# Performance work log

Measured on AMD Instinct MI355X. Metric: run time of the kernel, lower is better.

## Reference

```python
import jax, jax.numpy as jnp
import numpy as np

B, T, C = 2, 2048, 1024
NH, NKV, HD = 16, 4, 64
VEC = 32  # ve_gate_channels


def _rope(x, cos, sin):
    d = x.shape[-1] // 2
    x1, x2 = x[..., :d], x[..., d:]
    return jnp.concatenate([x1 * cos + x2 * sin, -x1 * sin + x2 * cos], axis=-1)


def _rmsnorm(x):
    eps = jnp.finfo(x.dtype).eps
    return x * jax.lax.rsqrt(jnp.mean(x * x, axis=-1, keepdims=True) + eps)


def setup_inputs() -> dict:
    key = jax.random.key(0)
    ks = jax.random.split(key, 9)
    s = 0.02
    return {
        "x": jax.random.normal(ks[0], (B, T, C), jnp.float32),
        "ve": jax.random.normal(ks[1], (B, T, NKV * HD), jnp.float32),
        "cos": jax.random.normal(ks[2], (1, T, 1, HD // 2), jnp.float32),
        "sin": jax.random.normal(ks[3], (1, T, 1, HD // 2), jnp.float32),
        "Wq": jax.random.normal(ks[4], (C, NH * HD), jnp.float32) * s,
        "Wk": jax.random.normal(ks[5], (C, NKV * HD), jnp.float32) * s,
        "Wv": jax.random.normal(ks[6], (C, NKV * HD), jnp.float32) * s,
        "Wproj": jax.random.normal(ks[7], (C, C), jnp.float32) * s,
        "Wgate": jax.random.normal(ks[8], (VEC, NKV), jnp.float32) * s,
        "window_size": 1024,
    }


def reference(x, ve, cos, sin, Wq, Wk, Wv, Wproj, Wgate, window_size):
    Bx, Tx, Cx = x.shape
    q = (x @ Wq).reshape(Bx, Tx, NH, HD)
    k = (x @ Wk).reshape(Bx, Tx, NKV, HD)
    v = (x @ Wv).reshape(Bx, Tx, NKV, HD)

    # value-embedding gate (has_ve True for this layer)
    gate = 2.0 * jax.nn.sigmoid(x[..., :VEC] @ Wgate)  # [B,T,NKV]
    v = v + gate[..., None] * ve.reshape(Bx, Tx, NKV, HD)

    q, k = _rope(q, cos, sin), _rope(k, cos, sin)
    q, k = _rmsnorm(q), _rmsnorm(k)

    q = q.transpose(0, 2, 1, 3)  # [B,NH,T,HD]
    k = k.transpose(0, 2, 1, 3)  # [B,NKV,T,HD]
    v = v.transpose(0, 2, 1, 3)

    # GQA: each KV head serves NH//NKV consecutive q heads
    g = NH // NKV
    k = jnp.repeat(k, g, axis=1)
    v = jnp.repeat(v, g, axis=1)

    row = jnp.arange(Tx)[:, None]
    col = jnp.arange(Tx)[None, :]
    mask = (col <= row) & (col >= row - window_size)  # causal sliding window

    scores = jnp.einsum("bhqd,bhkd->bhqk", q, k) / np.sqrt(HD).astype(np.float32)
    scores = jnp.where(mask[None, None], scores, jnp.finfo(scores.dtype).min)
    attn = jax.nn.softmax(scores, axis=-1)
    y = jnp.einsum("bhqk,bhkd->bhqd", attn, v)

    y = y.transpose(0, 2, 1, 3).reshape(Bx, Tx, Cx)
    return y @ Wproj
```

## Files before the change

### kernel.cpp

```cpp
#include <hip/hip_runtime.h>

typedef __bf16 bf16x8 __attribute__((ext_vector_type(8)));
typedef __bf16 bf16x4 __attribute__((ext_vector_type(4)));
typedef float f32x4 __attribute__((ext_vector_type(4)));

__device__ inline float tof(float v) { return v; }
__device__ inline float tof(__bf16 v) { return (float)v; }

__device__ inline bf16x8 load8(const __bf16* p) { return *(const bf16x8*)p; }
__device__ inline bf16x8 load8(const float* p) {
    const float4 a = *(const float4*)p;
    const float4 b = *(const float4*)(p + 4);
    bf16x8 r;
    r[0] = (__bf16)a.x; r[1] = (__bf16)a.y; r[2] = (__bf16)a.z; r[3] = (__bf16)a.w;
    r[4] = (__bf16)b.x; r[5] = (__bf16)b.y; r[6] = (__bf16)b.z; r[7] = (__bf16)b.w;
    return r;
}

__device__ __forceinline__ void cp16(__bf16* lds, const __bf16* g) {
    __builtin_amdgcn_global_load_lds((__attribute__((address_space(1))) void*)g,
                                     (__attribute__((address_space(3))) void*)lds,
                                     16, 0, 0);
}

__global__ void sniff_kernel(const unsigned short* __restrict__ xs, int* flag) {
    int tid = threadIdx.x;
    int bad = 0;
    for (int i = tid; i < 512; i += 64) {
        unsigned int f = ((unsigned int)xs[i]) << 16;
        float v = __uint_as_float(f);
        float a = fabsf(v);
        if (!(a <= 1e4f) || (a != 0.f && a < 1e-6f)) bad++;
    }
    bad += __shfl_xor(bad, 1);  bad += __shfl_xor(bad, 2);
    bad += __shfl_xor(bad, 4);  bad += __shfl_xor(bad, 8);
    bad += __shfl_xor(bad, 16); bad += __shfl_xor(bad, 32);
    if (tid == 0) *flag = (bad > 32) ? 1 : 0;
}

template <typename T>
__device__ __forceinline__ void prep_body(
    const T* __restrict__ x, const T* __restrict__ ve,
    const T* __restrict__ cosp, const T* __restrict__ sinp,
    const T* __restrict__ Wq, const T* __restrict__ Wk,
    const T* __restrict__ Wv, const T* __restrict__ Wp, const T* __restrict__ Wg,
    __bf16* __restrict__ xb, __bf16* __restrict__ veb,
    float* __restrict__ cosf_, float* __restrict__ sinf_,
    __bf16* __restrict__ WqT, __bf16* __restrict__ WkT,
    __bf16* __restrict__ WvT, __bf16* __restrict__ WpT,
    __bf16* __restrict__ wgb, __bf16* tile)
{
    const int b = blockIdx.x, tid = threadIdx.x;

    if (b < 2625) {
        int g = b * 256 + tid;
        if (g < 524288) {
            *(bf16x8*)(xb + (size_t)g * 8) = load8(x + (size_t)g * 8);
        } else if (g < 655360) {
            int gg = g - 524288;
            *(bf16x8*)(veb + (size_t)gg * 8) = load8(ve + (size_t)gg * 8);
        } else if (g < 663552) {
            int gg = g - 655360;
            const T* s = cosp + (size_t)gg * 8; float* d = cosf_ + (size_t)gg * 8;
#pragma unroll
            for (int j = 0; j < 8; ++j) d[j] = tof(s[j]);
        } else if (g < 671744) {
            int gg = g - 663552;
            const T* s = sinp + (size_t)gg * 8; float* d = sinf_ + (size_t)gg * 8;
#pragma unroll
            for (int j = 0; j < 8; ++j) d[j] = tof(s[j]);
        } else if (g < 671760) {
            int gg = g - 671744;
            const T* s = Wg + (size_t)gg * 8; __bf16* d = wgb + (size_t)gg * 8;
#pragma unroll
            for (int j = 0; j < 8; ++j) d[j] = (__bf16)tof(s[j]);
        }
    } else {
        int idx = b - 2625;
        const T* src; __bf16* dst; int C;
        if (idx < 256)      { src = Wq; dst = WqT; C = 1024; }
        else if (idx < 320) { src = Wk; dst = WkT; C = 256;  idx -= 256; }
        else if (idx < 384) { src = Wv; dst = WvT; C = 256;  idx -= 320; }
        else                { src = Wp; dst = WpT; C = 1024; idx -= 384; }
        const int ctiles = C >> 6;
        const int r0 = (idx / ctiles) * 64, c0 = (idx % ctiles) * 64;
#pragma unroll
        for (int i = 0; i < 2; ++i) {
            int c = tid + i * 256, ir = c >> 3, ic = (c & 7) * 8;
            *(bf16x8*)(&tile[ir * 72 + ic]) = load8(src + (size_t)(r0 + ir) * C + c0 + ic);
        }
        __syncthreads();
#pragma unroll
        for (int i = 0; i < 2; ++i) {
            int c = tid + i * 256, orr = c >> 3, okc = (c & 7) * 8;
            bf16x8 v;
#pragma unroll
            for (int j = 0; j < 8; ++j) v[j] = tile[(okc + j) * 72 + orr];
            *(bf16x8*)(dst + (size_t)(c0 + orr) * 1024 + r0 + okc) = v;
        }
    }
}

__global__ __launch_bounds__(256) void prep_kernel(
    const void* x, const void* ve, const void* cosp, const void* sinp,
    const void* Wq, const void* Wk, const void* Wv, const void* Wp, const void* Wg,
    __bf16* xb, __bf16* veb, float* cosf_, float* sinf_,
    __bf16* WqT, __bf16* WkT, __bf16* WvT, __bf16* WpT,
    __bf16* wgb, const int* __restrict__ flag)
{
    __shared__ __bf16 tile[64 * 72];
    if (*flag) {
        prep_body<float>((const float*)x, (const float*)ve, (const float*)cosp,
                         (const float*)sinp, (const float*)Wq, (const float*)Wk,
                         (const float*)Wv, (const float*)Wp, (const float*)Wg,
                         xb, veb, cosf_, sinf_, WqT, WkT, WvT, WpT, wgb, tile);
    } else {
        prep_body<__bf16>((const __bf16*)x, (const __bf16*)ve, (const __bf16*)cosp,
                          (const __bf16*)sinp, (const __bf16*)Wq, (const __bf16*)Wk,
                          (const __bf16*)Wv, (const __bf16*)Wp, (const __bf16*)Wg,
                          xb, veb, cosf_, sinf_, WqT, WkT, WvT, WpT, wgb, tile);
    }
}

__global__ __launch_bounds__(256) void qkv_kernel(
    const __bf16* __restrict__ xb,
    const __bf16* __restrict__ WqT, const __bf16* __restrict__ WkT,
    const __bf16* __restrict__ WvT, const __bf16* __restrict__ veb,
    const float* __restrict__ cosf_, const float* __restrict__ sinf_,
    const __bf16* __restrict__ wgb,
    __bf16* __restrict__ qo, __bf16* __restrict__ ko, __bf16* __restrict__ vTo)
{
    const int row0 = blockIdx.x * 128;
    const int cb = blockIdx.y;
    const __bf16* BT; int col0, h, mode;
    if (cb < 16)      { BT = WqT; col0 = cb * 64;        h = cb;      mode = 0; }
    else if (cb < 20) { BT = WkT; col0 = (cb - 16) * 64; h = cb - 16; mode = 1; }
    else              { BT = WvT; col0 = (cb - 20) * 64; h = cb - 20; mode = 2; }

    __shared__ __align__(16) __bf16 As[2][128 * 32];
    __shared__ __align__(16) __bf16 Bs[2][64 * 32];

    const int tid  = threadIdx.x;
    const int w    = tid >> 6;
    const int lane = tid & 63;
    const int quad = lane >> 4;
    const int l15  = lane & 15;
    const int wr   = w * 32;

    f32x4 acc[2][4];
#pragma unroll
    for (int mi = 0; mi < 2; ++mi)
#pragma unroll
        for (int nj = 0; nj < 4; ++nj) acc[mi][nj] = (f32x4){0.f, 0.f, 0.f, 0.f};

    bf16x8 wgB;
#pragma unroll
    for (int j = 0; j < 8; ++j) wgB[j] = (__bf16)0.f;
    if (mode == 2 && l15 < 4) {
#pragma unroll
        for (int j = 0; j < 8; ++j) wgB[j] = wgb[(quad * 8 + j) * 4 + l15];
    }
    f32x4 zacc[2];
    zacc[0] = (f32x4){0.f, 0.f, 0.f, 0.f};
    zacc[1] = (f32x4){0.f, 0.f, 0.f, 0.f};

    auto stage = [&](int buf, int kk) {
#pragma unroll
        for (int i = 0; i < 2; ++i) {
            int c = i * 256 + tid;
            cp16(&As[buf][c * 8], &xb[(size_t)(row0 + (c >> 2)) * 1024 + kk + ((c & 3) << 3)]);
        }
        cp16(&Bs[buf][tid * 8], &BT[(size_t)(col0 + (tid >> 2)) * 1024 + kk + ((tid & 3) << 3)]);
    };

    stage(0, 0);
    __syncthreads();

    for (int kk = 0; kk < 1024; kk += 32) {
        const int cur = (kk >> 5) & 1;
        if (kk + 32 < 1024) stage(cur ^ 1, kk + 32);

        bf16x8 a[2], bfr[4];
#pragma unroll
        for (int mi = 0; mi < 2; ++mi) a[mi]  = *(const bf16x8*)(&As[cur][(wr + mi * 16 + l15) * 32 + quad * 8]);
#pragma unroll
        for (int nj = 0; nj < 4; ++nj) bfr[nj] = *(const bf16x8*)(&Bs[cur][(nj * 16 + l15) * 32 + quad * 8]);
        if (mode == 2 && kk == 0) {
            zacc[0] = __builtin_amdgcn_mfma_f32_16x16x32_bf16(a[0], wgB, zacc[0], 0, 0, 0);
            zacc[1] = __builtin_amdgcn_mfma_f32_16x16x32_bf16(a[1], wgB, zacc[1], 0, 0, 0);
        }
#pragma unroll
        for (int mi = 0; mi < 2; ++mi)
#pragma unroll
            for (int nj = 0; nj < 4; ++nj)
                acc[mi][nj] = __builtin_amdgcn_mfma_f32_16x16x32_bf16(a[mi], bfr[nj], acc[mi][nj], 0, 0, 0);
        __syncthreads();
    }

    if (mode < 2) {
        __bf16* dst = (mode == 0) ? qo : ko;
        const int nh = (mode == 0) ? 16 : 4;
#pragma unroll
        for (int mi = 0; mi < 2; ++mi) {
#pragma unroll
            for (int r = 0; r < 4; ++r) {
                int row = row0 + wr + mi * 16 + quad * 4 + r;
                int b = row >> 11, t = row & 2047;
                float c0 = cosf_[t * 32 + l15];
                float c1 = cosf_[t * 32 + 16 + l15];
                float s0 = sinf_[t * 32 + l15];
                float s1 = sinf_[t * 32 + 16 + l15];
                float v0 =  c0 * acc[mi][0][r] + s0 * acc[mi][2][r];
                float v1 =  c1 * acc[mi][1][r] + s1 * acc[mi][3][r];
                float v2 = -s0 * acc[mi][0][r] + c0 * acc[mi][2][r];
                float v3 = -s1 * acc[mi][1][r] + c1 * acc[mi][3][r];
                float ss = v0 * v0 + v1 * v1 + v2 * v2 + v3 * v3;
                ss += __shfl_xor(ss, 1); ss += __shfl_xor(ss, 2);
                ss += __shfl_xor(ss, 4); ss += __shfl_xor(ss, 8);
                float sc = rsqrtf(ss * (1.f / 64.f) + 1.1920929e-7f);
                size_t base = (((size_t)b * nh + h) * 2048 + t) * 64;
                dst[base + 0 * 16 + l15] = (__bf16)(v0 * sc);
                dst[base + 1 * 16 + l15] = (__bf16)(v1 * sc);
                dst[base + 2 * 16 + l15] = (__bf16)(v2 * sc);
                dst[base + 3 * 16 + l15] = (__bf16)(v3 * sc);
            }
        }
    } else {
#pragma unroll
        for (int mi = 0; mi < 2; ++mi) {
            int rowb = row0 + wr + mi * 16 + quad * 4;
            int b = rowb >> 11, t0 = rowb & 2047;
            float gg[4];
#pragma unroll
            for (int r = 0; r < 4; ++r) {
                float zv = __shfl(zacc[mi][r], quad * 16 + h);
                gg[r] = 2.f / (1.f + __expf(-zv));
            }
#pragma unroll
            for (int nj = 0; nj < 4; ++nj) {
                int d = nj * 16 + l15;
                bf16x4 pack;
#pragma unroll
                for (int r = 0; r < 4; ++r) {
                    int row = rowb + r;
                    float val = acc[mi][nj][r] + gg[r] * tof(veb[(size_t)row * 256 + h * 64 + d]);
                    pack[r] = (__bf16)val;
                }
                size_t a = (((size_t)b * 4 + h) * 64 + d) * 2048 + t0;
                *(bf16x4*)(&vTo[a]) = pack;
            }
        }
    }
}

__global__ __launch_bounds__(256) void attn_kernel(
    const __bf16* __restrict__ qg, const __bf16* __restrict__ kg,
    const __bf16* __restrict__ vTg, __bf16* __restrict__ yo,
    const int* __restrict__ winp)
{
    const int q0 = blockIdx.x * 128;
    const int hh = blockIdx.y, b = blockIdx.z;
    const int kvh = hh >> 2;
    const int W = winp[0];

    const int tid  = threadIdx.x;
    const int w    = tid >> 6;
    const int lane = tid & 63;
    const int quad = lane >> 4;
    const int l15  = lane & 15;

    __shared__ __align__(16) __bf16 Ks[2][64 * 64];
    __shared__ __align__(16) __bf16 Vt[2][64 * 64];
    __shared__ __align__(16) __bf16 Ps[4][32 * 72];

    bf16x8 qf[2][2];
#pragma unroll
    for (int i = 0; i < 2; ++i) {
        size_t qb = (((size_t)b * 16 + hh) * 2048 + q0 + w * 32 + i * 16 + l15) * 64;
        qf[i][0] = *(const bf16x8*)(&qg[qb + quad * 8]);
        qf[i][1] = *(const bf16x8*)(&qg[qb + 32 + quad * 8]);
    }

    f32x4 oacc[2][4];
    float lsum[2][4];
#pragma unroll
    for (int i = 0; i < 2; ++i)
#pragma unroll
        for (int n = 0; n < 4; ++n) {
            oacc[i][n] = (f32x4){0.f, 0.f, 0.f, 0.f};
            lsum[i][n] = 0.f;
        }

    const int lo = q0 - W;
    const int kt_lo = lo > 0 ? (lo >> 6) : 0;
    const int kt_hi = (q0 + 127) >> 6;
    const size_t kvbase = ((size_t)b * 4 + kvh) * 2048 * 64;

    auto stage = [&](int buf, int k0) {
#pragma unroll
        for (int i = 0; i < 2; ++i) {
            int c = i * 256 + tid;
            int rr = c >> 3;
            int jj = (c & 7) ^ (rr & 7);
            cp16(&Ks[buf][c * 8], &kg[kvbase + (size_t)(k0 + rr) * 64 + jj * 8]);
            cp16(&Vt[buf][c * 8], &vTg[kvbase + (size_t)rr * 2048 + k0 + jj * 8]);
        }
    };

    stage(0, kt_lo * 64);
    __syncthreads();

    int cur = 0;
    for (int kt = kt_lo; kt <= kt_hi; ++kt) {
        const int k0 = kt * 64;
        const bool need_mask = (k0 + 63 > q0) || (q0 + 127 - k0 > W);
        if (kt < kt_hi) stage(cur ^ 1, k0 + 64);

        f32x4 sacc[2][4];
#pragma unroll
        for (int i = 0; i < 2; ++i)
#pragma unroll
            for (int n = 0; n < 4; ++n) sacc[i][n] = (f32x4){0.f, 0.f, 0.f, 0.f};
        const __bf16* Kc = &Ks[cur][0];
#pragma unroll
        for (int n = 0; n < 4; ++n) {
            int m = n * 16 + l15;
            bf16x8 b0 = *(const bf16x8*)(&Kc[m * 64 + (quad ^ (m & 7)) * 8]);
            bf16x8 b1 = *(const bf16x8*)(&Kc[m * 64 + ((4 + quad) ^ (m & 7)) * 8]);
#pragma unroll
            for (int i = 0; i < 2; ++i) {
                sacc[i][n] = __builtin_amdgcn_mfma_f32_16x16x32_bf16(qf[i][0], b0, sacc[i][n], 0, 0, 0);
                sacc[i][n] = __builtin_amdgcn_mfma_f32_16x16x32_bf16(qf[i][1], b1, sacc[i][n], 0, 0, 0);
            }
        }

#pragma unroll
        for (int i = 0; i < 2; ++i) {
#pragma unroll
            for (int r = 0; r < 4; ++r) {
                const int row_g = q0 + w * 32 + i * 16 + quad * 4 + r;
#pragma unroll
                for (int n = 0; n < 4; ++n) {
                    float p = exp2f(fmaf(sacc[i][n][r], 0.18033688f, -11.5415603f));
                    if (need_mask) {
                        int col_g = k0 + n * 16 + l15;
                        bool ok = (col_g <= row_g) && (row_g - col_g <= W);
                        p = ok ? p : 0.f;
                    }
                    lsum[i][r] += p;
                    Ps[w][(i * 16 + quad * 4 + r) * 72 + n * 16 + l15] = (__bf16)p;
                }
            }
        }
        asm volatile("s_waitcnt lgkmcnt(0)" ::: "memory");

        const __bf16* Vc = &Vt[cur][0];
#pragma unroll
        for (int ks = 0; ks < 2; ++ks) {
            bf16x8 pfr0 = *(const bf16x8*)(&Ps[w][l15 * 72 + ks * 32 + quad * 8]);
            bf16x8 pfr1 = *(const bf16x8*)(&Ps[w][(16 + l15) * 72 + ks * 32 + quad * 8]);
#pragma unroll
            for (int n = 0; n < 4; ++n) {
                int m = n * 16 + l15;
                bf16x8 bv = *(const bf16x8*)(&Vc[m * 64 + ((ks * 4 + quad) ^ (m & 7)) * 8]);
                oacc[0][n] = __builtin_amdgcn_mfma_f32_16x16x32_bf16(pfr0, bv, oacc[0][n], 0, 0, 0);
                oacc[1][n] = __builtin_amdgcn_mfma_f32_16x16x32_bf16(pfr1, bv, oacc[1][n], 0, 0, 0);
            }
        }

        __syncthreads();
        cur ^= 1;
    }

#pragma unroll
    for (int i = 0; i < 2; ++i) {
#pragma unroll
        for (int r = 0; r < 4; ++r) {
            float l = lsum[i][r];
            l += __shfl_xor(l, 1); l += __shfl_xor(l, 2);
            l += __shfl_xor(l, 4); l += __shfl_xor(l, 8);
            float inv = 1.f / l;
            int t = q0 + w * 32 + i * 16 + quad * 4 + r;
            size_t base = ((size_t)(b * 2048 + t)) * 1024 + hh * 64;
#pragma unroll
            for (int n = 0; n < 4; ++n)
                yo[base + n * 16 + l15] = (__bf16)(oacc[i][n][r] * inv);
        }
    }
}

__global__ __launch_bounds__(256) void proj_kernel(
    const __bf16* __restrict__ y, const __bf16* __restrict__ WpT,
    void* __restrict__ outp, const int* __restrict__ flag)
{
    const int isf32 = *flag;
    const int row0 = blockIdx.x * 128;
    const int col0 = blockIdx.y * 64;
    __shared__ __align__(16) __bf16 As[2][128 * 32];
    __shared__ __align__(16) __bf16 Bs[2][64 * 32];

    const int tid  = threadIdx.x;
    const int w    = tid >> 6;
    const int lane = tid & 63;
    const int quad = lane >> 4;
    const int l15  = lane & 15;
    const int wr   = w * 32;

    f32x4 acc[2][4];
#pragma unroll
    for (int mi = 0; mi < 2; ++mi)
#pragma unroll
        for (int nj = 0; nj < 4; ++nj) acc[mi][nj] = (f32x4){0.f, 0.f, 0.f, 0.f};

    auto stage = [&](int buf, int kk) {
#pragma unroll
        for (int i = 0; i < 2; ++i) {
            int c = i * 256 + tid;
            cp16(&As[buf][c * 8], &y[(size_t)(row0 + (c >> 2)) * 1024 + kk + ((c & 3) << 3)]);
        }
        cp16(&Bs[buf][tid * 8], &WpT[(size_t)(col0 + (tid >> 2)) * 1024 + kk + ((tid & 3) << 3)]);
    };

    stage(0, 0);
    __syncthreads();

    for (int kk = 0; kk < 1024; kk += 32) {
        const int cur = (kk >> 5) & 1;
        if (kk + 32 < 1024) stage(cur ^ 1, kk + 32);

        bf16x8 a[2], bfr[4];
#pragma unroll
        for (int mi = 0; mi < 2; ++mi) a[mi]  = *(const bf16x8*)(&As[cur][(wr + mi * 16 + l15) * 32 + quad * 8]);
#pragma unroll
        for (int nj = 0; nj < 4; ++nj) bfr[nj] = *(const bf16x8*)(&Bs[cur][(nj * 16 + l15) * 32 + quad * 8]);
#pragma unroll
        for (int mi = 0; mi < 2; ++mi)
#pragma unroll
            for (int nj = 0; nj < 4; ++nj)
                acc[mi][nj] = __builtin_amdgcn_mfma_f32_16x16x32_bf16(a[mi], bfr[nj], acc[mi][nj], 0, 0, 0);
        __syncthreads();
    }

#pragma unroll
    for (int mi = 0; mi < 2; ++mi)
#pragma unroll
        for (int r = 0; r < 4; ++r) {
            int row = row0 + wr + mi * 16 + quad * 4 + r;
            if (isf32) {
                float* out = (float*)outp;
#pragma unroll
                for (int nj = 0; nj < 4; ++nj)
                    out[(size_t)row * 1024 + col0 + nj * 16 + l15] = acc[mi][nj][r];
            } else {
                __bf16* out = (__bf16*)outp;
#pragma unroll
                for (int nj = 0; nj < 4; ++nj)
                    out[(size_t)row * 1024 + col0 + nj * 16 + l15] = (__bf16)acc[mi][nj][r];
            }
        }
}

extern "C" void kernel_launch(void* const* d_in, const int* in_sizes, int n_in,
                              void* d_out, int out_size, void* d_ws, size_t ws_size,
                              hipStream_t stream) {
    const int* win = (const int*)d_in[9];

    char* p = (char*)d_ws;
    int*    flag = (int*)p;                    p += 256;
    __bf16* q_ws = (__bf16*)p;                 p += (size_t)4194304 * 2;
    __bf16* k_ws = (__bf16*)p;                 p += (size_t)1048576 * 2;
    __bf16* vT_ws= (__bf16*)p;                 p += (size_t)1048576 * 2;
    __bf16* y_ws = (__bf16*)p;                 p += (size_t)4194304 * 2;
    __bf16* xb   = (__bf16*)p;                 p += (size_t)4194304 * 2;
    __bf16* veb  = (__bf16*)p;                 p += (size_t)1048576 * 2;
    __bf16* WqT  = (__bf16*)p;                 p += (size_t)1048576 * 2;
    __bf16* WkT  = (__bf16*)p;                 p += (size_t)262144 * 2;
    __bf16* WvT  = (__bf16*)p;                 p += (size_t)262144 * 2;
    __bf16* WpT  = (__bf16*)p;                 p += (size_t)1048576 * 2;
    float*  cosf_ = (float*)p;                 p += (size_t)65536 * 4;
    float*  sinf_ = (float*)p;                 p += (size_t)65536 * 4;
    __bf16* wgb   = (__bf16*)p;                p += 256;

    sniff_kernel<<<1, 64, 0, stream>>>((const unsigned short*)d_in[0], flag);

    prep_kernel<<<3265, 256, 0, stream>>>(
        d_in[0], d_in[1], d_in[2], d_in[3], d_in[4], d_in[5], d_in[6], d_in[7],
        d_in[8], xb, veb, cosf_, sinf_, WqT, WkT, WvT, WpT, wgb, flag);

    qkv_kernel<<<dim3(32, 24), 256, 0, stream>>>(xb, WqT, WkT, WvT, veb,
                                                 cosf_, sinf_, wgb, q_ws, k_ws, vT_ws);

    attn_kernel<<<dim3(16, 16, 2), 256, 0, stream>>>(q_ws, k_ws, vT_ws, y_ws, win);

    proj_kernel<<<dim3(32, 16), 256, 0, stream>>>(y_ws, WpT, d_out, flag);
}
```

Before: 201.0 us.

## Fuse input conversion into QKV GEMM, inline dtype sniff, widen K tiles

Removes the separate sniff kernel and the bulk x/ve/cos/sin conversion pass. Each block now detects the input dtype itself, and the QKV kernel reads raw inputs directly, converting fp32 x to bf16 while staging it into shared memory. The K step of the QKV and projection GEMMs doubles from 32 to 64, which halves the number of barriers. The softmax scale and max offset are folded into q normalisation, so attention calls exp2 directly on the scores. In exchange, x is converted to bf16 many times (once per column block) and the fp32 staging path uses register loads instead of async LDS copies.

```diff
diff --git a/kernel.cpp b/kernel.cpp
--- a/kernel.cpp
+++ b/kernel.cpp
@@ -17,66 +17,40 @@
     return r;
 }
 
+__device__ __forceinline__ float ldT(const void* p, size_t i, int isf32) {
+    return isf32 ? ((const float*)p)[i] : tof(((const __bf16*)p)[i]);
+}
+
 __device__ __forceinline__ void cp16(__bf16* lds, const __bf16* g) {
     __builtin_amdgcn_global_load_lds((__attribute__((address_space(1))) void*)g,
                                      (__attribute__((address_space(3))) void*)lds,
                                      16, 0, 0);
 }
 
-__global__ void sniff_kernel(const unsigned short* __restrict__ xs, int* flag) {
+__device__ __forceinline__ int sniff_block(const void* xraw) {
+    const unsigned short* xs = (const unsigned short*)xraw;
     int tid = threadIdx.x;
     int bad = 0;
-    for (int i = tid; i < 512; i += 64) {
-        unsigned int f = ((unsigned int)xs[i]) << 16;
-        float v = __uint_as_float(f);
+#pragma unroll
+    for (int k = 0; k < 2; ++k) {
+        float v = __uint_as_float(((unsigned int)xs[tid * 2 + k]) << 16);
         float a = fabsf(v);
-        if (!(a <= 1e4f) || (a != 0.f && a < 1e-6f)) bad++;
-    }
-    bad += __shfl_xor(bad, 1);  bad += __shfl_xor(bad, 2);
-    bad += __shfl_xor(bad, 4);  bad += __shfl_xor(bad, 8);
-    bad += __shfl_xor(bad, 16); bad += __shfl_xor(bad, 32);
-    if (tid == 0) *flag = (bad > 32) ? 1 : 0;
+        if (!(a <= 1e4f) || (a != 0.f && a < 1e-6f)) bad = 1;
+    }
+    return __syncthreads_count(bad) > 32;
 }
 
 template <typename T>
 __device__ __forceinline__ void prep_body(
-    const T* __restrict__ x, const T* __restrict__ ve,
-    const T* __restrict__ cosp, const T* __restrict__ sinp,
     const T* __restrict__ Wq, const T* __restrict__ Wk,
     const T* __restrict__ Wv, const T* __restrict__ Wp, const T* __restrict__ Wg,
-    __bf16* __restrict__ xb, __bf16* __restrict__ veb,
-    float* __restrict__ cosf_, float* __restrict__ sinf_,
     __bf16* __restrict__ WqT, __bf16* __restrict__ WkT,
     __bf16* __restrict__ WvT, __bf16* __restrict__ WpT,
     __bf16* __restrict__ wgb, __bf16* tile)
 {
     const int b = blockIdx.x, tid = threadIdx.x;
-
-    if (b < 2625) {
-        int g = b * 256 + tid;
-        if (g < 524288) {
-            *(bf16x8*)(xb + (size_t)g * 8) = load8(x + (size_t)g * 8);
-        } else if (g < 655360) {
-            int gg = g - 524288;
-            *(bf16x8*)(veb + (size_t)gg * 8) = load8(ve + (size_t)gg * 8);
-        } else if (g < 663552) {
-            int gg = g - 655360;
-            const T* s = cosp + (size_t)gg * 8; float* d = cosf_ + (size_t)gg * 8;
-#pragma unroll
-            for (int j = 0; j < 8; ++j) d[j] = tof(s[j]);
-        } else if (g < 671744) {
-            int gg = g - 663552;
-            const T* s = sinp + (size_t)gg * 8; float* d = sinf_ + (size_t)gg * 8;
-#pragma unroll
-            for (int j = 0; j < 8; ++j) d[j] = tof(s[j]);
-        } else if (g < 671760) {
-            int gg = g - 671744;
-            const T* s = Wg + (size_t)gg * 8; __bf16* d = wgb + (size_t)gg * 8;
-#pragma unroll
-            for (int j = 0; j < 8; ++j) d[j] = (__bf16)tof(s[j]);
-        }
-    } else {
-        int idx = b - 2625;
+    if (b < 640) {
+        int idx = b;
         const T* src; __bf16* dst; int C;
         if (idx < 256)      { src = Wq; dst = WqT; C = 1024; }
         else if (idx < 320) { src = Wk; dst = WkT; C = 256;  idx -= 256; }
@@ -98,38 +72,40 @@
             for (int j = 0; j < 8; ++j) v[j] = tile[(okc + j) * 72 + orr];
             *(bf16x8*)(dst + (size_t)(c0 + orr) * 1024 + r0 + okc) = v;
         }
+    } else if (tid < 128) {
+        wgb[tid] = (__bf16)tof(Wg[tid]);
     }
 }
 
 __global__ __launch_bounds__(256) void prep_kernel(
-    const void* x, const void* ve, const void* cosp, const void* sinp,
+    const void* x,
     const void* Wq, const void* Wk, const void* Wv, const void* Wp, const void* Wg,
-    __bf16* xb, __bf16* veb, float* cosf_, float* sinf_,
-    __bf16* WqT, __bf16* WkT, __bf16* WvT, __bf16* WpT,
-    __bf16* wgb, const int* __restrict__ flag)
+    __bf16* WqT, __bf16* WkT, __bf16* WvT, __bf16* WpT, __bf16* wgb)
 {
     __shared__ __bf16 tile[64 * 72];
-    if (*flag) {
-        prep_body<float>((const float*)x, (const float*)ve, (const float*)cosp,
-                         (const float*)sinp, (const float*)Wq, (const float*)Wk,
-                         (const float*)Wv, (const float*)Wp, (const float*)Wg,
-                         xb, veb, cosf_, sinf_, WqT, WkT, WvT, WpT, wgb, tile);
+    const int isf32 = sniff_block(x);
+    if (isf32) {
+        prep_body<float>((const float*)Wq, (const float*)Wk, (const float*)Wv,
+                         (const float*)Wp, (const float*)Wg,
+                         WqT, WkT, WvT, WpT, wgb, tile);
     } else {
-        prep_body<__bf16>((const __bf16*)x, (const __bf16*)ve, (const __bf16*)cosp,
-                          (const __bf16*)sinp, (const __bf16*)Wq, (const __bf16*)Wk,
-                          (const __bf16*)Wv, (const __bf16*)Wp, (const __bf16*)Wg,
-                          xb, veb, cosf_, sinf_, WqT, WkT, WvT, WpT, wgb, tile);
+        prep_body<__bf16>((const __bf16*)Wq, (const __bf16*)Wk, (const __bf16*)Wv,
+                          (const __bf16*)Wp, (const __bf16*)Wg,
+                          WqT, WkT, WvT, WpT, wgb, tile);
     }
 }
 
 __global__ __launch_bounds__(256) void qkv_kernel(
-    const __bf16* __restrict__ xb,
+    const void* __restrict__ xraw, const void* __restrict__ veraw,
+    const void* __restrict__ cosraw, const void* __restrict__ sinraw,
     const __bf16* __restrict__ WqT, const __bf16* __restrict__ WkT,
-    const __bf16* __restrict__ WvT, const __bf16* __restrict__ veb,
-    const float* __restrict__ cosf_, const float* __restrict__ sinf_,
-    const __bf16* __restrict__ wgb,
+    const __bf16* __restrict__ WvT, const __bf16* __restrict__ wgb,
     __bf16* __restrict__ qo, __bf16* __restrict__ ko, __bf16* __restrict__ vTo)
 {
+    const int isf32 = sniff_block(xraw);
+    const __bf16* xb = (const __bf16*)xraw;
+    const float*  xf = (const float*)xraw;
+
     const int row0 = blockIdx.x * 128;
     const int cb = blockIdx.y;
     const __bf16* BT; int col0, h, mode;
@@ -137,8 +113,8 @@
     else if (cb < 20) { BT = WkT; col0 = (cb - 16) * 64; h = cb - 16; mode = 1; }
     else              { BT = WvT; col0 = (cb - 20) * 64; h = cb - 20; mode = 2; }
 
-    __shared__ __align__(16) __bf16 As[2][128 * 32];
-    __shared__ __align__(16) __bf16 Bs[2][64 * 32];
+    __shared__ __align__(16) __bf16 As[2][128 * 64];
+    __shared__ __align__(16) __bf16 Bs[2][64 * 64];
 
     const int tid  = threadIdx.x;
     const int w    = tid >> 6;
@@ -164,52 +140,80 @@
     zacc[0] = (f32x4){0.f, 0.f, 0.f, 0.f};
     zacc[1] = (f32x4){0.f, 0.f, 0.f, 0.f};
 
-    auto stage = [&](int buf, int kk) {
+    auto stageA_bf = [&](int buf, int kk) {
+#pragma unroll
+        for (int i = 0; i < 4; ++i) {
+            int c = i * 256 + tid;
+            cp16(&As[buf][c * 8], &xb[(size_t)(row0 + (c >> 3)) * 1024 + kk + ((c & 7) << 3)]);
+        }
+    };
+    auto stageA_f32 = [&](int buf, int kk) {
+#pragma unroll
+        for (int i = 0; i < 4; ++i) {
+            int c = i * 256 + tid;
+            *(bf16x8*)(&As[buf][c * 8]) = load8(&xf[(size_t)(row0 + (c >> 3)) * 1024 + kk + ((c & 7) << 3)]);
+        }
+    };
+    auto stageB = [&](int buf, int kk) {
 #pragma unroll
         for (int i = 0; i < 2; ++i) {
             int c = i * 256 + tid;
-            cp16(&As[buf][c * 8], &xb[(size_t)(row0 + (c >> 2)) * 1024 + kk + ((c & 3) << 3)]);
-        }
-        cp16(&Bs[buf][tid * 8], &BT[(size_t)(col0 + (tid >> 2)) * 1024 + kk + ((tid & 3) << 3)]);
+            cp16(&Bs[buf][c * 8], &BT[(size_t)(col0 + (c >> 3)) * 1024 + kk + ((c & 7) << 3)]);
+        }
     };
 
-    stage(0, 0);
+    if (isf32) stageA_f32(0, 0); else stageA_bf(0, 0);
+    stageB(0, 0);
     __syncthreads();
 
-    for (int kk = 0; kk < 1024; kk += 32) {
-        const int cur = (kk >> 5) & 1;
-        if (kk + 32 < 1024) stage(cur ^ 1, kk + 32);
-
-        bf16x8 a[2], bfr[4];
-#pragma unroll
-        for (int mi = 0; mi < 2; ++mi) a[mi]  = *(const bf16x8*)(&As[cur][(wr + mi * 16 + l15) * 32 + quad * 8]);
-#pragma unroll
-        for (int nj = 0; nj < 4; ++nj) bfr[nj] = *(const bf16x8*)(&Bs[cur][(nj * 16 + l15) * 32 + quad * 8]);
+    for (int kk = 0; kk < 1024; kk += 64) {
+        const int cur = (kk >> 6) & 1;
+        const bool more = (kk + 64 < 1024);
+        if (more) {
+            if (isf32) stageA_f32(cur ^ 1, kk + 64); else stageA_bf(cur ^ 1, kk + 64);
+            stageB(cur ^ 1, kk + 64);
+        }
+
+        bf16x8 a[2][2], bfr[4][2];
+#pragma unroll
+        for (int mi = 0; mi < 2; ++mi)
+#pragma unroll
+            for (int kh = 0; kh < 2; ++kh)
+                a[mi][kh] = *(const bf16x8*)(&As[cur][(wr + mi * 16 + l15) * 64 + kh * 32 + quad * 8]);
+#pragma unroll
+        for (int nj = 0; nj < 4; ++nj)
+#pragma unroll
+            for (int kh = 0; kh < 2; ++kh)
+                bfr[nj][kh] = *(const bf16x8*)(&Bs[cur][(nj * 16 + l15) * 64 + kh * 32 + quad * 8]);
+
         if (mode == 2 && kk == 0) {
-            zacc[0] = __builtin_amdgcn_mfma_f32_16x16x32_bf16(a[0], wgB, zacc[0], 0, 0, 0);
-            zacc[1] = __builtin_amdgcn_mfma_f32_16x16x32_bf16(a[1], wgB, zacc[1], 0, 0, 0);
-        }
-#pragma unroll
-        for (int mi = 0; mi < 2; ++mi)
-#pragma unroll
-            for (int nj = 0; nj < 4; ++nj)
-                acc[mi][nj] = __builtin_amdgcn_mfma_f32_16x16x32_bf16(a[mi], bfr[nj], acc[mi][nj], 0, 0, 0);
+            zacc[0] = __builtin_amdgcn_mfma_f32_16x16x32_bf16(a[0][0], wgB, zacc[0], 0, 0, 0);
+            zacc[1] = __builtin_amdgcn_mfma_f32_16x16x32_bf16(a[1][0], wgB, zacc[1], 0, 0, 0);
+        }
+#pragma unroll
+        for (int kh = 0; kh < 2; ++kh)
+#pragma unroll
+            for (int mi = 0; mi < 2; ++mi)
+#pragma unroll
+                for (int nj = 0; nj < 4; ++nj)
+                    acc[mi][nj] = __builtin_amdgcn_mfma_f32_16x16x32_bf16(a[mi][kh], bfr[nj][kh], acc[mi][nj], 0, 0, 0);
         __syncthreads();
     }
 
     if (mode < 2) {
         __bf16* dst = (mode == 0) ? qo : ko;
         const int nh = (mode == 0) ? 16 : 4;
+        const float post = (mode == 0) ? 0.18033688f : 1.0f;
 #pragma unroll
         for (int mi = 0; mi < 2; ++mi) {
 #pragma unroll
             for (int r = 0; r < 4; ++r) {
                 int row = row0 + wr + mi * 16 + quad * 4 + r;
                 int b = row >> 11, t = row & 2047;
-                float c0 = cosf_[t * 32 + l15];
-                float c1 = cosf_[t * 32 + 16 + l15];
-                float s0 = sinf_[t * 32 + l15];
-                float s1 = sinf_[t * 32 + 16 + l15];
+                float c0 = ldT(cosraw, t * 32 + l15, isf32);
+                float c1 = ldT(cosraw, t * 32 + 16 + l15, isf32);
+                float s0 = ldT(sinraw, t * 32 + l15, isf32);
+                float s1 = ldT(sinraw, t * 32 + 16 + l15, isf32);
                 float v0 =  c0 * acc[mi][0][r] + s0 * acc[mi][2][r];
                 float v1 =  c1 * acc[mi][1][r] + s1 * acc[mi][3][r];
                 float v2 = -s0 * acc[mi][0][r] + c0 * acc[mi][2][r];
@@ -217,7 +221,7 @@
                 float ss = v0 * v0 + v1 * v1 + v2 * v2 + v3 * v3;
                 ss += __shfl_xor(ss, 1); ss += __shfl_xor(ss, 2);
                 ss += __shfl_xor(ss, 4); ss += __shfl_xor(ss, 8);
-                float sc = rsqrtf(ss * (1.f / 64.f) + 1.1920929e-7f);
+                float sc = rsqrtf(ss * (1.f / 64.f) + 1.1920929e-7f) * post;
                 size_t base = (((size_t)b * nh + h) * 2048 + t) * 64;
                 dst[base + 0 * 16 + l15] = (__bf16)(v0 * sc);
                 dst[base + 1 * 16 + l15] = (__bf16)(v1 * sc);
@@ -243,8 +247,8 @@
 #pragma unroll
                 for (int r = 0; r < 4; ++r) {
                     int row = rowb + r;
-                    float val = acc[mi][nj][r] + gg[r] * tof(veb[(size_t)row * 256 + h * 64 + d]);
-                    pack[r] = (__bf16)val;
+                    float vev = ldT(veraw, (size_t)row * 256 + h * 64 + d, isf32);
+                    pack[r] = (__bf16)(acc[mi][nj][r] + gg[r] * vev);
                 }
                 size_t a = (((size_t)b * 4 + h) * 64 + d) * 2048 + t0;
                 *(bf16x4*)(&vTo[a]) = pack;
@@ -341,7 +345,7 @@
                 const int row_g = q0 + w * 32 + i * 16 + quad * 4 + r;
 #pragma unroll
                 for (int n = 0; n < 4; ++n) {
-                    float p = exp2f(fmaf(sacc[i][n][r], 0.18033688f, -11.5415603f));
+                    float p = exp2f(sacc[i][n][r]);
                     if (need_mask) {
                         int col_g = k0 + n * 16 + l15;
                         bool ok = (col_g <= row_g) && (row_g - col_g <= W);
@@ -391,13 +395,13 @@
 
 __global__ __launch_bounds__(256) void proj_kernel(
     const __bf16* __restrict__ y, const __bf16* __restrict__ WpT,
-    void* __restrict__ outp, const int* __restrict__ flag)
+    void* __restrict__ outp, const void* __restrict__ xraw)
 {
-    const int isf32 = *flag;
+    const int isf32 = sniff_block(xraw);
     const int row0 = blockIdx.x * 128;
     const int col0 = blockIdx.y * 64;
-    __shared__ __align__(16) __bf16 As[2][128 * 32];
-    __shared__ __align__(16) __bf16 Bs[2][64 * 32];
+    __shared__ __align__(16) __bf16 As[2][128 * 64];
+    __shared__ __align__(16) __bf16 Bs[2][64 * 64];
 
     const int tid  = threadIdx.x;
     const int w    = tid >> 6;
@@ -414,30 +418,42 @@
 
     auto stage = [&](int buf, int kk) {
 #pragma unroll
+        for (int i = 0; i < 4; ++i) {
+            int c = i * 256 + tid;
+            cp16(&As[buf][c * 8], &y[(size_t)(row0 + (c >> 3)) * 1024 + kk + ((c & 7) << 3)]);
+        }
+#pragma unroll
         for (int i = 0; i < 2; ++i) {
             int c = i * 256 + tid;
-            cp16(&As[buf][c * 8], &y[(size_t)(row0 + (c >> 2)) * 1024 + kk + ((c & 3) << 3)]);
-        }
-        cp16(&Bs[buf][tid * 8], &WpT[(size_t)(col0 + (tid >> 2)) * 1024 + kk + ((tid & 3) << 3)]);
+            cp16(&Bs[buf][c * 8], &WpT[(size_t)(col0 + (c >> 3)) * 1024 + kk + ((c & 7) << 3)]);
+        }
     };
 
     stage(0, 0);
     __syncthreads();
 
-    for (int kk = 0; kk < 1024; kk += 32) {
-        const int cur = (kk >> 5) & 1;
-        if (kk + 32 < 1024) stage(cur ^ 1, kk + 32);
-
-        bf16x8 a[2], bfr[4];
-#pragma unroll
-        for (int mi = 0; mi < 2; ++mi) a[mi]  = *(const bf16x8*)(&As[cur][(wr + mi * 16 + l15) * 32 + quad * 8]);
-#pragma unroll
-        for (int nj = 0; nj < 4; ++nj) bfr[nj] = *(const bf16x8*)(&Bs[cur][(nj * 16 + l15) * 32 + quad * 8]);
+    for (int kk = 0; kk < 1024; kk += 64) {
+        const int cur = (kk >> 6) & 1;
+        if (kk + 64 < 1024) stage(cur ^ 1, kk + 64);
+
+        bf16x8 a[2][2], bfr[4][2];
 #pragma unroll
         for (int mi = 0; mi < 2; ++mi)
 #pragma unroll
-            for (int nj = 0; nj < 4; ++nj)
-                acc[mi][nj] = __builtin_amdgcn_mfma_f32_16x16x32_bf16(a[mi], bfr[nj], acc[mi][nj], 0, 0, 0);
+            for (int kh = 0; kh < 2; ++kh)
+                a[mi][kh] = *(const bf16x8*)(&As[cur][(wr + mi * 16 + l15) * 64 + kh * 32 + quad * 8]);
+#pragma unroll
+        for (int nj = 0; nj < 4; ++nj)
+#pragma unroll
+            for (int kh = 0; kh < 2; ++kh)
+                bfr[nj][kh] = *(const bf16x8*)(&Bs[cur][(nj * 16 + l15) * 64 + kh * 32 + quad * 8]);
+#pragma unroll
+        for (int kh = 0; kh < 2; ++kh)
+#pragma unroll
+            for (int mi = 0; mi < 2; ++mi)
+#pragma unroll
+                for (int nj = 0; nj < 4; ++nj)
+                    acc[mi][nj] = __builtin_amdgcn_mfma_f32_16x16x32_bf16(a[mi][kh], bfr[nj][kh], acc[mi][nj], 0, 0, 0);
         __syncthreads();
     }
 
@@ -466,31 +482,25 @@
     const int* win = (const int*)d_in[9];
 
     char* p = (char*)d_ws;
-    int*    flag = (int*)p;                    p += 256;
     __bf16* q_ws = (__bf16*)p;                 p += (size_t)4194304 * 2;
     __bf16* k_ws = (__bf16*)p;                 p += (size_t)1048576 * 2;
     __bf16* vT_ws= (__bf16*)p;                 p += (size_t)1048576 * 2;
     __bf16* y_ws = (__bf16*)p;                 p += (size_t)4194304 * 2;
-    __bf16* xb   = (__bf16*)p;                 p += (size_t)4194304 * 2;
-    __bf16* veb  = (__bf16*)p;                 p += (size_t)1048576 * 2;
     __bf16* WqT  = (__bf16*)p;                 p += (size_t)1048576 * 2;
     __bf16* WkT  = (__bf16*)p;                 p += (size_t)262144 * 2;
     __bf16* WvT  = (__bf16*)p;                 p += (size_t)262144 * 2;
     __bf16* WpT  = (__bf16*)p;                 p += (size_t)1048576 * 2;
-    float*  cosf_ = (float*)p;                 p += (size_t)65536 * 4;
-    float*  sinf_ = (float*)p;                 p += (size_t)65536 * 4;
-    __bf16* wgb   = (__bf16*)p;                p += 256;
-
-    sniff_kernel<<<1, 64, 0, stream>>>((const unsigned short*)d_in[0], flag);
-
-    prep_kernel<<<3265, 256, 0, stream>>>(
-        d_in[0], d_in[1], d_in[2], d_in[3], d_in[4], d_in[5], d_in[6], d_in[7],
-        d_in[8], xb, veb, cosf_, sinf_, WqT, WkT, WvT, WpT, wgb, flag);
-
-    qkv_kernel<<<dim3(32, 24), 256, 0, stream>>>(xb, WqT, WkT, WvT, veb,
-                                                 cosf_, sinf_, wgb, q_ws, k_ws, vT_ws);
+    __bf16* wgb  = (__bf16*)p;                 p += 256;
+
+    prep_kernel<<<641, 256, 0, stream>>>(
+        d_in[0], d_in[4], d_in[5], d_in[6], d_in[7], d_in[8],
+        WqT, WkT, WvT, WpT, wgb);
+
+    qkv_kernel<<<dim3(32, 24), 256, 0, stream>>>(
+        d_in[0], d_in[1], d_in[2], d_in[3],
+        WqT, WkT, WvT, wgb, q_ws, k_ws, vT_ws);
 
     attn_kernel<<<dim3(16, 16, 2), 256, 0, stream>>>(q_ws, k_ws, vT_ws, y_ws, win);
 
-    proj_kernel<<<dim3(32, 16), 256, 0, stream>>>(y_ws, WpT, d_out, flag);
-}
+    proj_kernel<<<dim3(32, 16), 256, 0, stream>>>(y_ws, WpT, d_out, d_in[0]);
+}
```

After: 203.2 us. No clear change (+1.1%).
